# Optimization experiments

Hardware: AMD Instinct MI355X
Metric: run time of the kernel (lower is better)

The kernel has to match this reference:

```python
import jax, jax.numpy as jnp
import numpy as np

N_NODES = 100000


def gcn_conv(x, W, b, src, dst, n):
    """PyG GCNConv: add self-loops, symmetric degree norm, linear, scatter-add."""
    loop = jnp.arange(n, dtype=src.dtype)
    s = jnp.concatenate([src, loop])  # source nodes (message origin)
    d = jnp.concatenate([dst, loop])  # target nodes (aggregation)
    deg = jax.ops.segment_sum(jnp.ones_like(d, dtype=x.dtype), d, num_segments=n)
    dinv = jnp.where(deg > 0, jax.lax.rsqrt(deg), 0.0)
    norm = dinv[s] * dinv[d]  # [E+N]
    h = x @ W  # [N, out]
    msg = h[s] * norm[:, None]  # [E+N, out]
    return jax.ops.segment_sum(msg, d, num_segments=n) + b


def setup_inputs() -> dict:
    key = jax.random.key(0)
    ks = jax.random.split(key, 8)
    n, e, din, dh, dout = N_NODES, 3200000, 128, 64, 6
    x = jax.random.normal(ks[0], (n, din), dtype=jnp.float32)
    edge_index = jax.random.randint(ks[1], (2, e), 0, n, dtype=jnp.int64)
    sc = lambda f: 1.0 / np.sqrt(f)
    W1 = jax.random.normal(ks[2], (din, dh), dtype=jnp.float32) * sc(din)
    b1 = jnp.zeros((dh,), dtype=jnp.float32)
    W2 = jax.random.normal(ks[3], (dh, dh), dtype=jnp.float32) * sc(dh)
    b2 = jnp.zeros((dh,), dtype=jnp.float32)
    W3 = jax.random.normal(ks[4], (dh, dout), dtype=jnp.float32) * sc(dh)
    b3 = jnp.zeros((dout,), dtype=jnp.float32)
    return {"x": x, "edge_index": edge_index, "W1": W1, "b1": b1,
            "W2": W2, "b2": b2, "W3": W3, "b3": b3}


def reference(x, edge_index, W1, b1, W2, b2, W3, b3):
    n = x.shape[0]
    src, dst = edge_index[0], edge_index[1]
    # eval mode: dropout is identity
    h = jax.nn.relu(gcn_conv(x, W1, b1, src, dst, n))
    h = jax.nn.relu(gcn_conv(h, W2, b2, src, dst, n))
    h = gcn_conv(h, W3, b3, src, dst, n)
    return jax.nn.log_softmax(h, axis=1)
```

## Files before the change

kernel.cpp:

```cpp
#include <hip/hip_runtime.h>
#include <hip/hip_fp16.h>
#include <math.h>


#define WS_ALIGN(x) (((x) + 255) & ~(size_t)255)
#define BKN 256
#define CAP 9216
#define EPT 8
#define BIN_THR 512
#define BIN_CHUNK (BIN_THR * EPT)

typedef _Float16 half8 __attribute__((ext_vector_type(8)));
typedef float floatx4 __attribute__((ext_vector_type(4)));

__global__ __launch_bounds__(512) void fat_bin_lin1_kernel(
    const int* __restrict__ src, const int* __restrict__ dst,
    int* __restrict__ cur, int* __restrict__ slab, int E, int NB, int binG,
    const float* __restrict__ Xf, const float* __restrict__ W1,
    _Float16* __restrict__ Y, int n) {
    __shared__ int smem[5632];
    const int tid = threadIdx.x;
    if (blockIdx.x < binG) {
        int* cnt   = smem;
        int* incl  = smem + 512;
        int* gbase = smem + 1024;
        int* stag  = smem + 1536;
        const int base = blockIdx.x * BIN_CHUNK + tid * EPT;
        cnt[tid] = 0;
        __syncthreads();
        int b[EPT], w[EPT], lp[EPT];
        #pragma unroll
        for (int k = 0; k < EPT; ++k) {
            int e = base + k;
            if (e < E) {
                int s = src[e], d = dst[e];
                b[k] = d >> 8;
                w[k] = (s << 8) | (d & 255);
            } else b[k] = -1;
        }
        #pragma unroll
        for (int k = 0; k < EPT; ++k)
            if (b[k] >= 0) lp[k] = atomicAdd(&cnt[b[k]], 1);
        __syncthreads();
        incl[tid] = cnt[tid];
        __syncthreads();
        for (int off = 1; off < 512; off <<= 1) {
            int v = 0;
            if (tid >= off) v = incl[tid - off];
            __syncthreads();
            incl[tid] += v;
            __syncthreads();
        }
        if (tid < NB) {
            int c = cnt[tid];
            gbase[tid] = c ? atomicAdd(&cur[tid], c) : 0;
        }
        #pragma unroll
        for (int k = 0; k < EPT; ++k)
            if (b[k] >= 0) stag[incl[b[k]] - cnt[b[k]] + lp[k]] = w[k];
        __syncthreads();
        const int total = incl[NB - 1];
        for (int idx = tid; idx < total; idx += BIN_THR) {
            int wv = stag[idx];
            int lo = 0, hi = NB - 1;
            while (lo < hi) { int mid = (lo + hi) >> 1; if (incl[mid] > idx) hi = mid; else lo = mid + 1; }
            int excl = incl[lo] - cnt[lo];
            int p = gbase[lo] + (idx - excl);
            if (p < CAP) slab[(size_t)lo * CAP + p] = wv;
        }
    } else {
        constexpr int K = 128, KC = 4;
        _Float16* Bf = (_Float16*)smem;
        for (int i = tid; i < KC * 4 * 64 * 8; i += 512) {
            int j = i & 7, lane = (i >> 3) & 63, tile = (i >> 9) & 3, kc = i >> 11;
            int k = kc * 32 + ((lane >> 4) << 3) + j;
            int col = tile * 16 + (lane & 15);
            Bf[i] = (_Float16)W1[k * 64 + col];
        }
        __syncthreads();
        const int lane = tid & 63, wid = tid >> 6;
        const int mrow = lane & 15, quad = lane >> 4;
        const int lblk = blockIdx.x - binG;
        #pragma unroll
        for (int tt = 0; tt < 2; ++tt) {
            const int base = lblk * 256 + wid * 32 + tt * 16;
            if (base >= n) continue;
            const int anode = min(base + mrow, n - 1);
            floatx4 acc[4] = {{0, 0, 0, 0}, {0, 0, 0, 0}, {0, 0, 0, 0}, {0, 0, 0, 0}};
            #pragma unroll
            for (int kc = 0; kc < KC; ++kc) {
                float4 xa = *(const float4*)&Xf[(size_t)anode * K + kc * 32 + quad * 8];
                float4 xb = *(const float4*)&Xf[(size_t)anode * K + kc * 32 + quad * 8 + 4];
                half8 a;
                a[0] = (_Float16)xa.x; a[1] = (_Float16)xa.y; a[2] = (_Float16)xa.z; a[3] = (_Float16)xa.w;
                a[4] = (_Float16)xb.x; a[5] = (_Float16)xb.y; a[6] = (_Float16)xb.z; a[7] = (_Float16)xb.w;
                #pragma unroll
                for (int t = 0; t < 4; ++t) {
                    half8 b = *(const half8*)&Bf[((kc * 4 + t) * 64 + lane) * 8];
                    acc[t] = __builtin_amdgcn_mfma_f32_16x16x32_f16(a, b, acc[t], 0, 0, 0);
                }
            }
            #pragma unroll
            for (int r = 0; r < 4; ++r) {
                int node = base + quad * 4 + r;
                if (node < n) {
                    #pragma unroll
                    for (int t = 0; t < 4; ++t)
                        Y[(size_t)node * 64 + t * 16 + mrow] = (_Float16)acc[t][r];
                }
            }
        }
    }
}

__global__ __launch_bounds__(512) void bucket_sort_kernel(
    const int* __restrict__ slab, const int* __restrict__ cur,
    int* __restrict__ srcS, int2* __restrict__ rows,
    float* __restrict__ dinv, int n) {
    __shared__ int cnt[BKN], s[BKN], cursor[BKN];
    const int b = blockIdx.x, tid = threadIdx.x;
    const int m = min(cur[b], CAP);
    const int* sp = slab + (size_t)b * CAP;
    if (tid < BKN) cnt[tid] = 0;
    __syncthreads();
    for (int j = tid; j < m; j += 512) atomicAdd(&cnt[sp[j] & (BKN - 1)], 1);
    __syncthreads();
    if (tid < BKN) s[tid] = cnt[tid];
    __syncthreads();
    for (int off = 1; off < BKN; off <<= 1) {
        int v = 0;
        if (tid < BKN && tid >= off) v = s[tid - off];
        __syncthreads();
        if (tid < BKN) s[tid] += v;
        __syncthreads();
    }
    if (tid < BKN) {
        int ofs = s[tid] - cnt[tid];
        cursor[tid] = ofs;
        int node = b * BKN + tid;
        if (node < n) {
            rows[node] = make_int2(b * CAP + ofs, b * CAP + ofs + cnt[tid]);
            dinv[node] = rsqrtf((float)(cnt[tid] + 1));
        }
    }
    __syncthreads();
    for (int j = tid; j < m; j += 512) {
        int w = sp[j];
        int p = atomicAdd(&cursor[w & (BKN - 1)], 1);
        srcS[(size_t)b * CAP + p] = w >> 8;
    }
}

__global__ __launch_bounds__(256) void linear_mfma_f16_kernel(
    const _Float16* __restrict__ Xh, const float* __restrict__ W,
    const float* __restrict__ dinv, _Float16* __restrict__ Y, int n) {
    constexpr int K = 64, KC = 2;
    __shared__ _Float16 Bf[KC * 4 * 64 * 8];
    const int tid = threadIdx.x;
    for (int i = tid; i < KC * 4 * 64 * 8; i += 256) {
        int j = i & 7, lane = (i >> 3) & 63, tile = (i >> 9) & 3, kc = i >> 11;
        int k = kc * 32 + ((lane >> 4) << 3) + j;
        int col = tile * 16 + (lane & 15);
        Bf[i] = (_Float16)W[k * 64 + col];
    }
    __syncthreads();
    const int lane = tid & 63, wid = tid >> 6;
    const int mrow = lane & 15, quad = lane >> 4;
    #pragma unroll
    for (int tt = 0; tt < 4; ++tt) {
        const int base = (blockIdx.x * 4 + tt) * 64 + wid * 16;
        if (base >= n) continue;
        const int anode = min(base + mrow, n - 1);
        floatx4 acc[4] = {{0, 0, 0, 0}, {0, 0, 0, 0}, {0, 0, 0, 0}, {0, 0, 0, 0}};
        #pragma unroll
        for (int kc = 0; kc < KC; ++kc) {
            half8 a = *(const half8*)&Xh[(size_t)anode * K + kc * 32 + quad * 8];
            #pragma unroll
            for (int t = 0; t < 4; ++t) {
                half8 b = *(const half8*)&Bf[((kc * 4 + t) * 64 + lane) * 8];
                acc[t] = __builtin_amdgcn_mfma_f32_16x16x32_f16(a, b, acc[t], 0, 0, 0);
            }
        }
        #pragma unroll
        for (int r = 0; r < 4; ++r) {
            int node = base + quad * 4 + r;
            if (node < n) {
                float di = dinv[node];
                #pragma unroll
                for (int t = 0; t < 4; ++t)
                    Y[(size_t)node * 64 + t * 16 + mrow] = (_Float16)(acc[t][r] * di);
            }
        }
    }
}

__global__ __launch_bounds__(256) void agg64s_kernel(
    const _Float16* __restrict__ H1, const float* __restrict__ dinv,
    const int* __restrict__ srcS, const int2* __restrict__ rows,
    const float* __restrict__ bias, _Float16* __restrict__ Out, int n) {
    const int wave = (blockIdx.x * blockDim.x + threadIdx.x) >> 6;
    const int lane = threadIdx.x & 63;
    if (wave >= n) return;
    const int slot = lane >> 3;
    const int f8 = lane & 7;
    const int2 row = rows[wave];
    const int beg = row.x, end = row.y;
    half8 hA, hB;
    #pragma unroll
    for (int i = 0; i < 8; ++i) { hA[i] = (_Float16)0.f; hB[i] = (_Float16)0.f; }
    int j = beg;
    for (; j + 32 <= end; j += 32) {
        int s0 = srcS[j      + slot];
        int s1 = srcS[j + 8  + slot];
        int s2 = srcS[j + 16 + slot];
        int s3 = srcS[j + 24 + slot];
        _Float16 d0 = (_Float16)dinv[s0];
        _Float16 d1 = (_Float16)dinv[s1];
        _Float16 d2 = (_Float16)dinv[s2];
        _Float16 d3 = (_Float16)dinv[s3];
        half8 v0 = *(const half8*)&H1[(size_t)s0 * 64 + f8 * 8];
        half8 v1 = *(const half8*)&H1[(size_t)s1 * 64 + f8 * 8];
        half8 v2 = *(const half8*)&H1[(size_t)s2 * 64 + f8 * 8];
        half8 v3 = *(const half8*)&H1[(size_t)s3 * 64 + f8 * 8];
        hA += v0 * d0; hB += v1 * d1; hA += v2 * d2; hB += v3 * d3;
    }
    for (; j + 16 <= end; j += 16) {
        int s0 = srcS[j + slot];
        int s1 = srcS[j + 8 + slot];
        _Float16 d0 = (_Float16)dinv[s0];
        _Float16 d1 = (_Float16)dinv[s1];
        half8 v0 = *(const half8*)&H1[(size_t)s0 * 64 + f8 * 8];
        half8 v1 = *(const half8*)&H1[(size_t)s1 * 64 + f8 * 8];
        hA += v0 * d0; hB += v1 * d1;
    }
    for (; j < end; j += 8) {
        int jj = j + slot;
        if (jj < end) {
            int s0 = srcS[jj];
            _Float16 d0 = (_Float16)dinv[s0];
            half8 v = *(const half8*)&H1[(size_t)s0 * 64 + f8 * 8];
            hA += v * d0;
        }
    }
    half8 ht = hA + hB;
    #pragma unroll
    for (int mask = 8; mask <= 32; mask <<= 1) {
        int4 ci = *(int4*)&ht, oi;
        oi.x = __shfl_xor(ci.x, mask);
        oi.y = __shfl_xor(ci.y, mask);
        oi.z = __shfl_xor(ci.z, mask);
        oi.w = __shfl_xor(ci.w, mask);
        ht += *(half8*)&oi;
    }
    half8 self = *(const half8*)&H1[(size_t)wave * 64 + f8 * 8];
    const float di = dinv[wave];
    float4 b0 = *(const float4*)&bias[f8 * 8];
    float4 b1v = *(const float4*)&bias[f8 * 8 + 4];
    float bb[8] = {b0.x, b0.y, b0.z, b0.w, b1v.x, b1v.y, b1v.z, b1v.w};
    half8 o;
    #pragma unroll
    for (int i = 0; i < 8; ++i) {
        float t = ((float)ht[i] + di * (float)self[i]) * di + bb[i];
        o[i] = (_Float16)fmaxf(t, 0.f);
    }
    if (slot == 0) *(half8*)&Out[(size_t)wave * 64 + f8 * 8] = o;
}

__global__ __launch_bounds__(256) void agg64w3_kernel(
    const _Float16* __restrict__ Hs, const float* __restrict__ dinv,
    const int* __restrict__ srcS, const int2* __restrict__ rows,
    const float* __restrict__ bias, const float* __restrict__ W3,
    __half* __restrict__ Yc, int n) {
    __shared__ float W3l[64 * 6];
    const int tid = threadIdx.x;
    for (int i = tid; i < 64 * 6; i += 256) W3l[i] = W3[i];
    __syncthreads();
    const int wave = (blockIdx.x * blockDim.x + tid) >> 6;
    const int lane = tid & 63;
    if (wave >= n) return;
    const int slot = lane >> 3;
    const int f8 = lane & 7;
    const int2 row = rows[wave];
    const int beg = row.x, end = row.y;
    half8 hA, hB;
    #pragma unroll
    for (int i = 0; i < 8; ++i) { hA[i] = (_Float16)0.f; hB[i] = (_Float16)0.f; }
    int j = beg;
    for (; j + 32 <= end; j += 32) {
        int s0 = srcS[j      + slot];
        int s1 = srcS[j + 8  + slot];
        int s2 = srcS[j + 16 + slot];
        int s3 = srcS[j + 24 + slot];
        half8 v0 = *(const half8*)&Hs[(size_t)s0 * 64 + f8 * 8];
        half8 v1 = *(const half8*)&Hs[(size_t)s1 * 64 + f8 * 8];
        half8 v2 = *(const half8*)&Hs[(size_t)s2 * 64 + f8 * 8];
        half8 v3 = *(const half8*)&Hs[(size_t)s3 * 64 + f8 * 8];
        hA += v0; hB += v1; hA += v2; hB += v3;
    }
    for (; j + 16 <= end; j += 16) {
        int s0 = srcS[j + slot];
        int s1 = srcS[j + 8 + slot];
        half8 v0 = *(const half8*)&Hs[(size_t)s0 * 64 + f8 * 8];
        half8 v1 = *(const half8*)&Hs[(size_t)s1 * 64 + f8 * 8];
        hA += v0; hB += v1;
    }
    for (; j < end; j += 8) {
        int jj = j + slot;
        if (jj < end) {
            half8 v = *(const half8*)&Hs[(size_t)srcS[jj] * 64 + f8 * 8];
            hA += v;
        }
    }
    half8 ht = hA + hB;
    #pragma unroll
    for (int mask = 8; mask <= 32; mask <<= 1) {
        int4 ci = *(int4*)&ht, oi;
        oi.x = __shfl_xor(ci.x, mask);
        oi.y = __shfl_xor(ci.y, mask);
        oi.z = __shfl_xor(ci.z, mask);
        oi.w = __shfl_xor(ci.w, mask);
        ht += *(half8*)&oi;
    }
    half8 self = *(const half8*)&Hs[(size_t)wave * 64 + f8 * 8];
    const float di = dinv[wave];
    float4 b0 = *(const float4*)&bias[f8 * 8];
    float4 b1v = *(const float4*)&bias[f8 * 8 + 4];
    float bb[8] = {b0.x, b0.y, b0.z, b0.w, b1v.x, b1v.y, b1v.z, b1v.w};
    float p[6] = {0.f, 0.f, 0.f, 0.f, 0.f, 0.f};
    #pragma unroll
    for (int i = 0; i < 8; ++i) {
        float h2 = fmaxf(((float)ht[i] + (float)self[i]) * di + bb[i], 0.f);
        const float* wr = &W3l[(f8 * 8 + i) * 6];
        #pragma unroll
        for (int q = 0; q < 6; ++q) p[q] = fmaf(h2, wr[q], p[q]);
    }
    #pragma unroll
    for (int mask = 1; mask <= 4; mask <<= 1) {
        #pragma unroll
        for (int q = 0; q < 6; ++q) p[q] += __shfl_xor(p[q], mask);
    }
    if (lane == 0) {
        half8 o;
        #pragma unroll
        for (int q = 0; q < 6; ++q) o[q] = (_Float16)(p[q] * di);
        o[6] = (_Float16)0.f; o[7] = (_Float16)0.f;
        *(half8*)&Yc[(size_t)wave * 8] = o;
    }
}

__global__ __launch_bounds__(256) void agg6_lsm_kernel(
    const _Float16* __restrict__ Hs6, const float* __restrict__ dinv,
    const int* __restrict__ srcS, const int2* __restrict__ rows,
    const float* __restrict__ bias, float* __restrict__ out, int n) {
    const int wave = (blockIdx.x * blockDim.x + threadIdx.x) >> 6;
    const int lane = threadIdx.x & 63;
    if (wave >= n) return;
    const int2 row = rows[wave];
    const int beg = row.x, end = row.y;
    half8 ht;
    #pragma unroll
    for (int i = 0; i < 8; ++i) ht[i] = (_Float16)0.f;
    for (int j = beg + lane; j < end; j += 64) {
        int s = srcS[j];
        ht += *(const half8*)&Hs6[(size_t)s * 8];
    }
    #pragma unroll
    for (int mask = 1; mask <= 32; mask <<= 1) {
        int4 ci = *(int4*)&ht, oi;
        oi.x = __shfl_xor(ci.x, mask);
        oi.y = __shfl_xor(ci.y, mask);
        oi.z = __shfl_xor(ci.z, mask);
        oi.w = __shfl_xor(ci.w, mask);
        ht += *(half8*)&oi;
    }
    half8 self = *(const half8*)&Hs6[(size_t)wave * 8];
    const float di = dinv[wave];
    float a[6];
    #pragma unroll
    for (int q = 0; q < 6; ++q)
        a[q] = ((float)ht[q] + (float)self[q]) * di + bias[q];
    float mx = a[0];
    #pragma unroll
    for (int q = 1; q < 6; ++q) mx = fmaxf(mx, a[q]);
    float sum = 0.f;
    #pragma unroll
    for (int q = 0; q < 6; ++q) sum += expf(a[q] - mx);
    float lse = mx + logf(sum);
    if (lane == 0) {
        float* op = &out[(size_t)wave * 6];
        *(float2*)(op)     = make_float2(a[0] - lse, a[1] - lse);
        *(float2*)(op + 2) = make_float2(a[2] - lse, a[3] - lse);
        *(float2*)(op + 4) = make_float2(a[4] - lse, a[5] - lse);
    }
}

extern "C" void kernel_launch(void* const* d_in, const int* in_sizes, int n_in,
                              void* d_out, int out_size, void* d_ws, size_t ws_size,
                              hipStream_t stream) {
    const float* x  = (const float*)d_in[0];
    const int*   ei = (const int*)d_in[1];
    const float* W1 = (const float*)d_in[2];
    const float* b1 = (const float*)d_in[3];
    const float* W2 = (const float*)d_in[4];
    const float* b2 = (const float*)d_in[5];
    const float* W3 = (const float*)d_in[6];
    const float* b3 = (const float*)d_in[7];
    float* out = (float*)d_out;

    const int n = in_sizes[0] / 128;
    const int E = in_sizes[1] / 2;
    const int* src = ei;
    const int* dst = ei + E;
    const int NB = (n + BKN - 1) / BKN;

    char* ws = (char*)d_ws;
    auto carve = [&](size_t bytes) { char* p = ws; ws += WS_ALIGN(bytes); return p; };
    int*      cur  = (int*)     carve((size_t)NB * 4);
    float*    dinv = (float*)   carve((size_t)n * 4);
    int*      slab = (int*)     carve((size_t)NB * CAP * 4);
    int*      srcS = (int*)     carve((size_t)NB * CAP * 4);
    int2*     rows = (int2*)    carve((size_t)n * 8);
    _Float16* hsA  = (_Float16*)carve((size_t)n * 64 * 2 + 4096);
    _Float16* hsB  = (_Float16*)carve((size_t)n * 64 * 2 + 4096);
    _Float16* hsC  = (_Float16*)carve((size_t)n * 8 * 2);
    (void)ws_size; (void)n_in; (void)out_size;

    const int binG = (E + BIN_CHUNK - 1) / BIN_CHUNK;
    const int linG = (n + 255) / 256;
    const int aggGrid = (n + 3) / 4;

    (void)hipMemsetAsync(cur, 0, (size_t)NB * 4, stream);
    fat_bin_lin1_kernel<<<binG + linG, 512, 0, stream>>>(
        src, dst, cur, slab, E, NB, binG, x, W1, hsA, n);

    bucket_sort_kernel<<<NB, 512, 0, stream>>>(slab, cur, srcS, rows, dinv, n);

    agg64s_kernel<<<aggGrid, 256, 0, stream>>>(hsA, dinv, srcS, rows, b1, hsB, n);

    linear_mfma_f16_kernel<<<(n + 255) / 256, 256, 0, stream>>>(hsB, W2, dinv, hsA, n);

    agg64w3_kernel<<<aggGrid, 256, 0, stream>>>(hsA, dinv, srcS, rows, b2, W3, (__half*)hsC, n);

    agg6_lsm_kernel<<<aggGrid, 256, 0, stream>>>(hsC, dinv, srcS, rows, b3, out, n);
}
```

Before: 344.5 us.

## Split layer-1 linear across bin and bucket-sort kernels; use fp16 dot2 in W3 epilogue

Moves half of the layer-1 linear blocks from the binning kernel into the bucket-sort kernel. The bucket sort runs only a few hundred blocks and would otherwise underfill the GPU, so the extra work fills idle CUs. Separately, the agg64w3 epilogue now does bias, scale and ReLU in packed half precision and computes the 64x6 projection with fdot2 on half2 weights staged in shared memory. This cuts ALU work but lowers the precision of the intermediate values.

Result: no change. 343.0 us (-0.4%).

```diff
diff --git a/kernel.cpp b/kernel.cpp
--- a/kernel.cpp
+++ b/kernel.cpp
@@ -11,7 +11,52 @@
 #define BIN_CHUNK (BIN_THR * EPT)
 
 typedef _Float16 half8 __attribute__((ext_vector_type(8)));
+typedef _Float16 half2v __attribute__((ext_vector_type(2)));
 typedef float floatx4 __attribute__((ext_vector_type(4)));
+
+__device__ __forceinline__ void lin1_role(
+    const float* __restrict__ Xf, const float* __restrict__ W1,
+    _Float16* __restrict__ Y, int n, int lblk, int tid, _Float16* Bf) {
+    constexpr int K = 128, KC = 4;
+    for (int i = tid; i < KC * 4 * 64 * 8; i += 512) {
+        int j = i & 7, lane = (i >> 3) & 63, tile = (i >> 9) & 3, kc = i >> 11;
+        int k = kc * 32 + ((lane >> 4) << 3) + j;
+        int col = tile * 16 + (lane & 15);
+        Bf[i] = (_Float16)W1[k * 64 + col];
+    }
+    __syncthreads();
+    const int lane = tid & 63, wid = tid >> 6;
+    const int mrow = lane & 15, quad = lane >> 4;
+    #pragma unroll
+    for (int tt = 0; tt < 2; ++tt) {
+        const int base = lblk * 256 + wid * 32 + tt * 16;
+        if (base >= n) continue;
+        const int anode = min(base + mrow, n - 1);
+        floatx4 acc[4] = {{0, 0, 0, 0}, {0, 0, 0, 0}, {0, 0, 0, 0}, {0, 0, 0, 0}};
+        #pragma unroll
+        for (int kc = 0; kc < KC; ++kc) {
+            float4 xa = *(const float4*)&Xf[(size_t)anode * K + kc * 32 + quad * 8];
+            float4 xb = *(const float4*)&Xf[(size_t)anode * K + kc * 32 + quad * 8 + 4];
+            half8 a;
+            a[0] = (_Float16)xa.x; a[1] = (_Float16)xa.y; a[2] = (_Float16)xa.z; a[3] = (_Float16)xa.w;
+            a[4] = (_Float16)xb.x; a[5] = (_Float16)xb.y; a[6] = (_Float16)xb.z; a[7] = (_Float16)xb.w;
+            #pragma unroll
+            for (int t = 0; t < 4; ++t) {
+                half8 b = *(const half8*)&Bf[((kc * 4 + t) * 64 + lane) * 8];
+                acc[t] = __builtin_amdgcn_mfma_f32_16x16x32_f16(a, b, acc[t], 0, 0, 0);
+            }
+        }
+        #pragma unroll
+        for (int r = 0; r < 4; ++r) {
+            int node = base + quad * 4 + r;
+            if (node < n) {
+                #pragma unroll
+                for (int t = 0; t < 4; ++t)
+                    Y[(size_t)node * 64 + t * 16 + mrow] = (_Float16)acc[t][r];
+            }
+        }
+    }
+}
 
 __global__ __launch_bounds__(512) void fat_bin_lin1_kernel(
     const int* __restrict__ src, const int* __restrict__ dst,
@@ -69,85 +114,55 @@
             if (p < CAP) slab[(size_t)lo * CAP + p] = wv;
         }
     } else {
-        constexpr int K = 128, KC = 4;
-        _Float16* Bf = (_Float16*)smem;
-        for (int i = tid; i < KC * 4 * 64 * 8; i += 512) {
-            int j = i & 7, lane = (i >> 3) & 63, tile = (i >> 9) & 3, kc = i >> 11;
-            int k = kc * 32 + ((lane >> 4) << 3) + j;
-            int col = tile * 16 + (lane & 15);
-            Bf[i] = (_Float16)W1[k * 64 + col];
-        }
-        __syncthreads();
-        const int lane = tid & 63, wid = tid >> 6;
-        const int mrow = lane & 15, quad = lane >> 4;
-        const int lblk = blockIdx.x - binG;
-        #pragma unroll
-        for (int tt = 0; tt < 2; ++tt) {
-            const int base = lblk * 256 + wid * 32 + tt * 16;
-            if (base >= n) continue;
-            const int anode = min(base + mrow, n - 1);
-            floatx4 acc[4] = {{0, 0, 0, 0}, {0, 0, 0, 0}, {0, 0, 0, 0}, {0, 0, 0, 0}};
-            #pragma unroll
-            for (int kc = 0; kc < KC; ++kc) {
-                float4 xa = *(const float4*)&Xf[(size_t)anode * K + kc * 32 + quad * 8];
-                float4 xb = *(const float4*)&Xf[(size_t)anode * K + kc * 32 + quad * 8 + 4];
-                half8 a;
-                a[0] = (_Float16)xa.x; a[1] = (_Float16)xa.y; a[2] = (_Float16)xa.z; a[3] = (_Float16)xa.w;
-                a[4] = (_Float16)xb.x; a[5] = (_Float16)xb.y; a[6] = (_Float16)xb.z; a[7] = (_Float16)xb.w;
-                #pragma unroll
-                for (int t = 0; t < 4; ++t) {
-                    half8 b = *(const half8*)&Bf[((kc * 4 + t) * 64 + lane) * 8];
-                    acc[t] = __builtin_amdgcn_mfma_f32_16x16x32_f16(a, b, acc[t], 0, 0, 0);
-                }
-            }
-            #pragma unroll
-            for (int r = 0; r < 4; ++r) {
-                int node = base + quad * 4 + r;
-                if (node < n) {
-                    #pragma unroll
-                    for (int t = 0; t < 4; ++t)
-                        Y[(size_t)node * 64 + t * 16 + mrow] = (_Float16)acc[t][r];
-                }
-            }
-        }
-    }
-}
-
-__global__ __launch_bounds__(512) void bucket_sort_kernel(
+        lin1_role(Xf, W1, Y, n, blockIdx.x - binG, tid, (_Float16*)smem);
+    }
+}
+
+__global__ __launch_bounds__(512) void fat_bucket_lin1_kernel(
     const int* __restrict__ slab, const int* __restrict__ cur,
     int* __restrict__ srcS, int2* __restrict__ rows,
-    float* __restrict__ dinv, int n) {
-    __shared__ int cnt[BKN], s[BKN], cursor[BKN];
-    const int b = blockIdx.x, tid = threadIdx.x;
-    const int m = min(cur[b], CAP);
-    const int* sp = slab + (size_t)b * CAP;
-    if (tid < BKN) cnt[tid] = 0;
-    __syncthreads();
-    for (int j = tid; j < m; j += 512) atomicAdd(&cnt[sp[j] & (BKN - 1)], 1);
-    __syncthreads();
-    if (tid < BKN) s[tid] = cnt[tid];
-    __syncthreads();
-    for (int off = 1; off < BKN; off <<= 1) {
-        int v = 0;
-        if (tid < BKN && tid >= off) v = s[tid - off];
-        __syncthreads();
-        if (tid < BKN) s[tid] += v;
-        __syncthreads();
-    }
-    if (tid < BKN) {
-        int ofs = s[tid] - cnt[tid];
-        cursor[tid] = ofs;
-        int node = b * BKN + tid;
-        if (node < n) {
-            rows[node] = make_int2(b * CAP + ofs, b * CAP + ofs + cnt[tid]);
-            dinv[node] = rsqrtf((float)(cnt[tid] + 1));
-        }
-    }
-    __syncthreads();
-    for (int j = tid; j < m; j += 512) {
-        int w = sp[j];
-        int p = atomicAdd(&cursor[w & (BKN - 1)], 1);
-        srcS[(size_t)b * CAP + p] = w >> 8;
+    float* __restrict__ dinv, int NB, int linBase,
+    const float* __restrict__ Xf, const float* __restrict__ W1,
+    _Float16* __restrict__ Y, int n) {
+    __shared__ int smem[4096];
+    const int tid = threadIdx.x;
+    if ((int)blockIdx.x < NB) {
+        int* cnt    = smem;
+        int* s      = smem + 256;
+        int* cursor = smem + 512;
+        const int b = blockIdx.x;
+        const int m = min(cur[b], CAP);
+        const int* sp = slab + (size_t)b * CAP;
+        if (tid < BKN) cnt[tid] = 0;
+        __syncthreads();
+        for (int j = tid; j < m; j += 512) atomicAdd(&cnt[sp[j] & (BKN - 1)], 1);
+        __syncthreads();
+        if (tid < BKN) s[tid] = cnt[tid];
+        __syncthreads();
+        for (int off = 1; off < BKN; off <<= 1) {
+            int v = 0;
+            if (tid < BKN && tid >= off) v = s[tid - off];
+            __syncthreads();
+            if (tid < BKN) s[tid] += v;
+            __syncthreads();
+        }
+        if (tid < BKN) {
+            int ofs = s[tid] - cnt[tid];
+            cursor[tid] = ofs;
+            int node = b * BKN + tid;
+            if (node < n) {
+                rows[node] = make_int2(b * CAP + ofs, b * CAP + ofs + cnt[tid]);
+                dinv[node] = rsqrtf((float)(cnt[tid] + 1));
+            }
+        }
+        __syncthreads();
+        for (int j = tid; j < m; j += 512) {
+            int w = sp[j];
+            int p = atomicAdd(&cursor[w & (BKN - 1)], 1);
+            srcS[(size_t)b * CAP + p] = w >> 8;
+        }
+    } else {
+        lin1_role(Xf, W1, Y, n, (int)blockIdx.x - NB + linBase, tid, (_Float16*)smem);
     }
 }
 
@@ -271,9 +286,22 @@
     const int* __restrict__ srcS, const int2* __restrict__ rows,
     const float* __restrict__ bias, const float* __restrict__ W3,
     __half* __restrict__ Yc, int n) {
-    __shared__ float W3l[64 * 6];
+    __shared__ unsigned int W3h[6 * 32];
+    __shared__ unsigned int B2h[32];
     const int tid = threadIdx.x;
-    for (int i = tid; i < 64 * 6; i += 256) W3l[i] = W3[i];
+    for (int i = tid; i < 6 * 32; i += 256) {
+        int q = i >> 5, jp = i & 31;
+        half2v v;
+        v[0] = (_Float16)W3[(2 * jp) * 6 + q];
+        v[1] = (_Float16)W3[(2 * jp + 1) * 6 + q];
+        W3h[i] = *(unsigned int*)&v;
+    }
+    if (tid < 32) {
+        half2v v;
+        v[0] = (_Float16)bias[2 * tid];
+        v[1] = (_Float16)bias[2 * tid + 1];
+        B2h[tid] = *(unsigned int*)&v;
+    }
     __syncthreads();
     const int wave = (blockIdx.x * blockDim.x + tid) >> 6;
     const int lane = tid & 63;
@@ -323,16 +351,33 @@
     }
     half8 self = *(const half8*)&Hs[(size_t)wave * 64 + f8 * 8];
     const float di = dinv[wave];
-    float4 b0 = *(const float4*)&bias[f8 * 8];
-    float4 b1v = *(const float4*)&bias[f8 * 8 + 4];
-    float bb[8] = {b0.x, b0.y, b0.z, b0.w, b1v.x, b1v.y, b1v.z, b1v.w};
-    float p[6] = {0.f, 0.f, 0.f, 0.f, 0.f, 0.f};
-    #pragma unroll
-    for (int i = 0; i < 8; ++i) {
-        float h2 = fmaxf(((float)ht[i] + (float)self[i]) * di + bb[i], 0.f);
-        const float* wr = &W3l[(f8 * 8 + i) * 6];
-        #pragma unroll
-        for (int q = 0; q < 6; ++q) p[q] = fmaf(h2, wr[q], p[q]);
+    half8 bb8 = *(half8*)&B2h[f8 * 4];
+    half8 s8 = ht + self;
+    half8 t8 = s8 * (_Float16)di + bb8;
+    half8 h2;
+    #pragma unroll
+    for (int i = 0; i < 8; ++i) h2[i] = t8[i] > (_Float16)0.f ? t8[i] : (_Float16)0.f;
+    float p[6];
+    #pragma unroll
+    for (int q = 0; q < 6; ++q) {
+        float acc = 0.f;
+        #pragma unroll
+        for (int t = 0; t < 4; ++t) {
+            half2v hp;
+            hp[0] = h2[2 * t]; hp[1] = h2[2 * t + 1];
+            unsigned int wu = W3h[q * 32 + f8 * 4 + t];
+            half2v wv = *(half2v*)&wu;
+#if defined(__has_builtin)
+#if __has_builtin(__builtin_amdgcn_fdot2)
+            acc = __builtin_amdgcn_fdot2(hp, wv, acc, false);
+#else
+            acc += (float)hp[0] * (float)wv[0] + (float)hp[1] * (float)wv[1];
+#endif
+#else
+            acc += (float)hp[0] * (float)wv[0] + (float)hp[1] * (float)wv[1];
+#endif
+        }
+        p[q] = acc;
     }
     #pragma unroll
     for (int mask = 1; mask <= 4; mask <<= 1) {
@@ -427,13 +472,16 @@
 
     const int binG = (E + BIN_CHUNK - 1) / BIN_CHUNK;
     const int linG = (n + 255) / 256;
+    const int linA = (linG + 1) / 2;
+    const int linB = linG - linA;
     const int aggGrid = (n + 3) / 4;
 
     (void)hipMemsetAsync(cur, 0, (size_t)NB * 4, stream);
-    fat_bin_lin1_kernel<<<binG + linG, 512, 0, stream>>>(
+    fat_bin_lin1_kernel<<<binG + linA, 512, 0, stream>>>(
         src, dst, cur, slab, E, NB, binG, x, W1, hsA, n);
 
-    bucket_sort_kernel<<<NB, 512, 0, stream>>>(slab, cur, srcS, rows, dinv, n);
+    fat_bucket_lin1_kernel<<<NB + linB, 512, 0, stream>>>(
+        slab, cur, srcS, rows, dinv, NB, linA, x, W1, hsA, n);
 
     agg64s_kernel<<<aggGrid, 256, 0, stream>>>(hsA, dinv, srcS, rows, b1, hsB, n);
 
```

## Aggregate before layer-2 linear and fuse W2 and W3 matmuls into one kernel

Applied to the files above, without the earlier changes.

Uses linearity to reorder layer 2 so that aggregation, A·(dinv·h), runs before the W2 multiply. The W2 MFMA, bias, ReLU and the W3 projection are then fused into one kernel that stages h2 in LDS and does a second MFMA for the 6 output columns. The separate linear kernel and the W3 epilogue inside the aggregation are removed, and the aggregation kernel becomes a plain gather-sum. The layer-2 aggregation still gathers 64-wide fp16 rows, so the gather traffic is unchanged. The change adds block-level syncs and LDS traffic in the fused kernel, and h2 is rounded to fp16 before the W3 multiply.

After: 331.4 us. 1.04x faster.

```diff
diff --git a/kernel.cpp b/kernel.cpp
--- a/kernel.cpp
+++ b/kernel.cpp
@@ -11,6 +11,7 @@
 #define BIN_CHUNK (BIN_THR * EPT)
 
 typedef _Float16 half8 __attribute__((ext_vector_type(8)));
+typedef _Float16 half2v __attribute__((ext_vector_type(2)));
 typedef float floatx4 __attribute__((ext_vector_type(4)));
 
 __global__ __launch_bounds__(512) void fat_bin_lin1_kernel(
@@ -151,49 +152,6 @@
     }
 }
 
-__global__ __launch_bounds__(256) void linear_mfma_f16_kernel(
-    const _Float16* __restrict__ Xh, const float* __restrict__ W,
-    const float* __restrict__ dinv, _Float16* __restrict__ Y, int n) {
-    constexpr int K = 64, KC = 2;
-    __shared__ _Float16 Bf[KC * 4 * 64 * 8];
-    const int tid = threadIdx.x;
-    for (int i = tid; i < KC * 4 * 64 * 8; i += 256) {
-        int j = i & 7, lane = (i >> 3) & 63, tile = (i >> 9) & 3, kc = i >> 11;
-        int k = kc * 32 + ((lane >> 4) << 3) + j;
-        int col = tile * 16 + (lane & 15);
-        Bf[i] = (_Float16)W[k * 64 + col];
-    }
-    __syncthreads();
-    const int lane = tid & 63, wid = tid >> 6;
-    const int mrow = lane & 15, quad = lane >> 4;
-    #pragma unroll
-    for (int tt = 0; tt < 4; ++tt) {
-        const int base = (blockIdx.x * 4 + tt) * 64 + wid * 16;
-        if (base >= n) continue;
-        const int anode = min(base + mrow, n - 1);
-        floatx4 acc[4] = {{0, 0, 0, 0}, {0, 0, 0, 0}, {0, 0, 0, 0}, {0, 0, 0, 0}};
-        #pragma unroll
-        for (int kc = 0; kc < KC; ++kc) {
-            half8 a = *(const half8*)&Xh[(size_t)anode * K + kc * 32 + quad * 8];
-            #pragma unroll
-            for (int t = 0; t < 4; ++t) {
-                half8 b = *(const half8*)&Bf[((kc * 4 + t) * 64 + lane) * 8];
-                acc[t] = __builtin_amdgcn_mfma_f32_16x16x32_f16(a, b, acc[t], 0, 0, 0);
-            }
-        }
-        #pragma unroll
-        for (int r = 0; r < 4; ++r) {
-            int node = base + quad * 4 + r;
-            if (node < n) {
-                float di = dinv[node];
-                #pragma unroll
-                for (int t = 0; t < 4; ++t)
-                    Y[(size_t)node * 64 + t * 16 + mrow] = (_Float16)(acc[t][r] * di);
-            }
-        }
-    }
-}
-
 __global__ __launch_bounds__(256) void agg64s_kernel(
     const _Float16* __restrict__ H1, const float* __restrict__ dinv,
     const int* __restrict__ srcS, const int2* __restrict__ rows,
@@ -261,22 +219,17 @@
     #pragma unroll
     for (int i = 0; i < 8; ++i) {
         float t = ((float)ht[i] + di * (float)self[i]) * di + bb[i];
-        o[i] = (_Float16)fmaxf(t, 0.f);
+        o[i] = (_Float16)(fmaxf(t, 0.f) * di);
     }
     if (slot == 0) *(half8*)&Out[(size_t)wave * 64 + f8 * 8] = o;
 }
 
-__global__ __launch_bounds__(256) void agg64w3_kernel(
+__global__ __launch_bounds__(256) void aggU_kernel(
     const _Float16* __restrict__ Hs, const float* __restrict__ dinv,
     const int* __restrict__ srcS, const int2* __restrict__ rows,
-    const float* __restrict__ bias, const float* __restrict__ W3,
-    __half* __restrict__ Yc, int n) {
-    __shared__ float W3l[64 * 6];
-    const int tid = threadIdx.x;
-    for (int i = tid; i < 64 * 6; i += 256) W3l[i] = W3[i];
-    __syncthreads();
-    const int wave = (blockIdx.x * blockDim.x + tid) >> 6;
-    const int lane = tid & 63;
+    _Float16* __restrict__ Out, int n) {
+    const int wave = (blockIdx.x * blockDim.x + threadIdx.x) >> 6;
+    const int lane = threadIdx.x & 63;
     if (wave >= n) return;
     const int slot = lane >> 3;
     const int f8 = lane & 7;
@@ -323,28 +276,79 @@
     }
     half8 self = *(const half8*)&Hs[(size_t)wave * 64 + f8 * 8];
     const float di = dinv[wave];
-    float4 b0 = *(const float4*)&bias[f8 * 8];
-    float4 b1v = *(const float4*)&bias[f8 * 8 + 4];
-    float bb[8] = {b0.x, b0.y, b0.z, b0.w, b1v.x, b1v.y, b1v.z, b1v.w};
-    float p[6] = {0.f, 0.f, 0.f, 0.f, 0.f, 0.f};
-    #pragma unroll
-    for (int i = 0; i < 8; ++i) {
-        float h2 = fmaxf(((float)ht[i] + (float)self[i]) * di + bb[i], 0.f);
-        const float* wr = &W3l[(f8 * 8 + i) * 6];
-        #pragma unroll
-        for (int q = 0; q < 6; ++q) p[q] = fmaf(h2, wr[q], p[q]);
-    }
-    #pragma unroll
-    for (int mask = 1; mask <= 4; mask <<= 1) {
-        #pragma unroll
-        for (int q = 0; q < 6; ++q) p[q] += __shfl_xor(p[q], mask);
-    }
-    if (lane == 0) {
-        half8 o;
-        #pragma unroll
-        for (int q = 0; q < 6; ++q) o[q] = (_Float16)(p[q] * di);
-        o[6] = (_Float16)0.f; o[7] = (_Float16)0.f;
-        *(half8*)&Yc[(size_t)wave * 8] = o;
+    half8 o;
+    #pragma unroll
+    for (int i = 0; i < 8; ++i)
+        o[i] = (_Float16)(((float)ht[i] + (float)self[i]) * di);
+    if (slot == 0) *(half8*)&Out[(size_t)wave * 64 + f8 * 8] = o;
+}
+
+__global__ __launch_bounds__(256) void lin23_kernel(
+    const _Float16* __restrict__ U, const float* __restrict__ W2,
+    const float* __restrict__ b2, const float* __restrict__ W3,
+    const float* __restrict__ dinv, __half* __restrict__ Yc, int n) {
+    constexpr int K = 64, KC = 2;
+    __shared__ _Float16 Bf[KC * 4 * 64 * 8];
+    __shared__ _Float16 BW3[KC * 64 * 8];
+    __shared__ _Float16 h2L[64][72];
+    __shared__ float b2L[64];
+    const int tid = threadIdx.x;
+    for (int i = tid; i < KC * 4 * 64 * 8; i += 256) {
+        int j = i & 7, lane = (i >> 3) & 63, tile = (i >> 9) & 3, kc = i >> 11;
+        int k = kc * 32 + ((lane >> 4) << 3) + j;
+        int col = tile * 16 + (lane & 15);
+        Bf[i] = (_Float16)W2[k * 64 + col];
+    }
+    for (int i = tid; i < KC * 64 * 8; i += 256) {
+        int j = i & 7, lane = (i >> 3) & 63, kc = i >> 9;
+        int k = kc * 32 + ((lane >> 4) << 3) + j;
+        int col = lane & 15;
+        BW3[i] = (col < 6) ? (_Float16)W3[k * 6 + col] : (_Float16)0.f;
+    }
+    if (tid < 64) b2L[tid] = b2[tid];
+    __syncthreads();
+    const int lane = tid & 63, wid = tid >> 6;
+    const int mrow = lane & 15, quad = lane >> 4;
+    for (int tt = 0; tt < 4; ++tt) {
+        const int base = (blockIdx.x * 4 + tt) * 64 + wid * 16;
+        const int anode = min(base + mrow, n - 1);
+        floatx4 acc[4] = {{0, 0, 0, 0}, {0, 0, 0, 0}, {0, 0, 0, 0}, {0, 0, 0, 0}};
+        #pragma unroll
+        for (int kc = 0; kc < KC; ++kc) {
+            half8 a = *(const half8*)&U[(size_t)anode * K + kc * 32 + quad * 8];
+            #pragma unroll
+            for (int t = 0; t < 4; ++t) {
+                half8 b = *(const half8*)&Bf[((kc * 4 + t) * 64 + lane) * 8];
+                acc[t] = __builtin_amdgcn_mfma_f32_16x16x32_f16(a, b, acc[t], 0, 0, 0);
+            }
+        }
+        #pragma unroll
+        for (int r = 0; r < 4; ++r) {
+            int nl = wid * 16 + quad * 4 + r;
+            #pragma unroll
+            for (int t = 0; t < 4; ++t) {
+                int f = t * 16 + mrow;
+                h2L[nl][f] = (_Float16)fmaxf(acc[t][r] + b2L[f], 0.f);
+            }
+        }
+        __syncthreads();
+        floatx4 acc2 = {0, 0, 0, 0};
+        #pragma unroll
+        for (int kc = 0; kc < KC; ++kc) {
+            half8 a2 = *(const half8*)&h2L[wid * 16 + mrow][kc * 32 + quad * 8];
+            half8 b3f = *(const half8*)&BW3[(kc * 64 + lane) * 8];
+            acc2 = __builtin_amdgcn_mfma_f32_16x16x32_f16(a2, b3f, acc2, 0, 0, 0);
+        }
+        const int q = lane & 15;
+        #pragma unroll
+        for (int r = 0; r < 4; ++r) {
+            int node = base + quad * 4 + r;
+            if (node < n && q < 8) {
+                float v = (q < 6) ? acc2[r] * dinv[node] : 0.f;
+                Yc[(size_t)node * 8 + q] = __float2half_rn(v);
+            }
+        }
+        __syncthreads();
     }
 }
 
@@ -437,9 +441,9 @@
 
     agg64s_kernel<<<aggGrid, 256, 0, stream>>>(hsA, dinv, srcS, rows, b1, hsB, n);
 
-    linear_mfma_f16_kernel<<<(n + 255) / 256, 256, 0, stream>>>(hsB, W2, dinv, hsA, n);
-
-    agg64w3_kernel<<<aggGrid, 256, 0, stream>>>(hsA, dinv, srcS, rows, b2, W3, (__half*)hsC, n);
+    aggU_kernel<<<aggGrid, 256, 0, stream>>>(hsB, dinv, srcS, rows, hsA, n);
+
+    lin23_kernel<<<linG, 256, 0, stream>>>(hsA, W2, b2, W3, dinv, (__half*)hsC, n);
 
     agg6_lsm_kernel<<<aggGrid, 256, 0, stream>>>(hsC, dinv, srcS, rows, b3, out, n);
 }
```
